# Kernel optimization log

Measured on AMD Instinct MI355X. Metric: run time of the kernel, lower is better.

Reference implementation:

```python
import jax, jax.numpy as jnp
import numpy as np

LATENT = 64
COND = 768
HEADS = 8
R = 8           # LoRA rank
SCALING = 1.0   # lora_alpha / r
SCALE = (LATENT / HEADS) ** -0.5


def _lora_linear(x, W, b, A, B):
    # loralib-style: y = x W^T + b + scaling * (x A^T) B^T
    return x @ W.T + b + SCALING * ((x @ A.T) @ B.T)


def setup_inputs() -> dict:
    key = jax.random.key(0)
    ks = jax.random.split(key, 20)
    B, C, H, W_ = 16, LATENT, 64, 64
    L = 77
    z = jax.random.normal(ks[0], (B, C, H, W_), dtype=jnp.float32)
    cond = jax.random.normal(ks[1], (B, L, COND), dtype=jnp.float32)

    def lin(k, out_d, in_d):
        k1, k2, k3 = jax.random.split(k, 3)
        W = jax.random.normal(k1, (out_d, in_d), dtype=jnp.float32) * 0.02
        b = jnp.zeros((out_d,), dtype=jnp.float32)
        A = jax.random.normal(k2, (R, in_d), dtype=jnp.float32) * 0.02
        Bm = jax.random.normal(k3, (out_d, R), dtype=jnp.float32) * 0.02
        return W, b, A, Bm

    Wq, bq, Aq, Bq = lin(ks[2], LATENT, LATENT)
    Wk, bk, Ak, Bk = lin(ks[3], LATENT, COND)
    Wv, bv, Av, Bv = lin(ks[4], LATENT, COND)
    Wo, bo, Ao, Bo = lin(ks[5], LATENT, LATENT)
    return dict(z=z, cond=cond,
                Wq=Wq, bq=bq, Aq=Aq, Bq=Bq,
                Wk=Wk, bk=bk, Ak=Ak, Bk=Bk,
                Wv=Wv, bv=bv, Av=Av, Bv=Bv,
                Wo=Wo, bo=bo, Ao=Ao, Bo=Bo)


def reference(z, cond, Wq, bq, Aq, Bq, Wk, bk, Ak, Bk, Wv, bv, Av, Bv, Wo, bo, Ao, Bo):
    B, C, H, W_ = z.shape
    hw = H * W_
    dh = C // HEADS
    z_flat = z.transpose(0, 2, 3, 1).reshape(B, hw, C)  # [B, hw, C]

    q = _lora_linear(z_flat, Wq, bq, Aq, Bq)   # [B, hw, C]
    k = _lora_linear(cond, Wk, bk, Ak, Bk)     # [B, L, C]
    v = _lora_linear(cond, Wv, bv, Av, Bv)     # [B, L, C]

    q = q.reshape(B, hw, HEADS, dh).transpose(0, 2, 1, 3)  # [B, h, hw, dh]
    k = k.reshape(B, -1, HEADS, dh).transpose(0, 2, 1, 3)  # [B, h, L, dh]
    v = v.reshape(B, -1, HEADS, dh).transpose(0, 2, 1, 3)

    dots = jnp.einsum('bhqd,bhkd->bhqk', q, k) * SCALE  # [B, h, hw, L]
    attn = jax.nn.softmax(dots, axis=-1)
    out = jnp.einsum('bhqk,bhkd->bhqd', attn, v)        # [B, h, hw, dh]
    out = out.transpose(0, 2, 1, 3).reshape(B, hw, C)
    out = _lora_linear(out, Wo, bo, Ao, Bo)
    return out.reshape(B, H, W_, C).transpose(0, 3, 1, 2)  # [B, C, H, W]
```

## Files before the change

### kernel.cpp

```cpp
#include <hip/hip_runtime.h>


#define HW   4096
#define CHN  64
#define LSEQ 77
#define CD   768
#define NB   16

#define OFF_WQ 0
#define OFF_WK 4096
#define OFF_WV 53248
#define OFF_WO 102400
#define OFF_K  106496
#define OFF_V  185344
#define OFF_PA 264192

#define QF 0.51011784563163f

__global__ __launch_bounds__(256) void prep_weights(
    const float* __restrict__ Wq, const float* __restrict__ Aq, const float* __restrict__ Bq,
    const float* __restrict__ Wk, const float* __restrict__ Ak, const float* __restrict__ Bk,
    const float* __restrict__ Wv, const float* __restrict__ Av, const float* __restrict__ Bv,
    const float* __restrict__ Wo, const float* __restrict__ Ao, const float* __restrict__ Bo,
    float* __restrict__ ws) {
  int idx = blockIdx.x * 256 + threadIdx.x;
  const float *W, *A, *Bm;
  float* out;
  int in_d, local;
  float scale = 1.0f;
  if (idx < 4096)        { W = Wq; A = Aq; Bm = Bq; out = ws + OFF_WQ; in_d = 64;  local = idx; scale = QF; }
  else if (idx < 53248)  { W = Wk; A = Ak; Bm = Bk; out = ws + OFF_WK; in_d = 768; local = idx - 4096; }
  else if (idx < 102400) { W = Wv; A = Av; Bm = Bv; out = ws + OFF_WV; in_d = 768; local = idx - 53248; }
  else                   { W = Wo; A = Ao; Bm = Bo; out = ws + OFF_WO; in_d = 64;  local = idx - 102400; }
  int co = local & 63;
  int c  = local >> 6;
  float val = W[co * in_d + c];
  #pragma unroll
  for (int r = 0; r < 8; r++) val += Bm[co * 8 + r] * A[r * in_d + c];
  out[local] = val * scale;
}

__global__ __launch_bounds__(128, 2) void kvproj(
    const float* __restrict__ cond,
    const float* __restrict__ wkT,
    const float* __restrict__ wvT,
    float* __restrict__ part) {
  int chunk = blockIdx.x;
  int kv    = blockIdx.y;
  int b     = blockIdx.z;
  int l     = threadIdx.x;
  if (l >= LSEQ) return;
  const float* wT = kv ? wvT : wkT;
  int c0 = chunk * 64;
  const float* xr = cond + (b * LSEQ + l) * CD + c0;
  float zr[64];
  #pragma unroll
  for (int i = 0; i < 16; i++) {
    float4 t4 = ((const float4*)xr)[i];
    zr[4*i] = t4.x; zr[4*i+1] = t4.y; zr[4*i+2] = t4.z; zr[4*i+3] = t4.w;
  }
  float acc[64];
  #pragma unroll
  for (int co = 0; co < 64; co++) acc[co] = 0.f;
  #pragma unroll 4
  for (int c = 0; c < 64; c++) {
    float zv = zr[c];
    #pragma unroll
    for (int co = 0; co < 64; co++) acc[co] = fmaf(zv, wT[(c0 + c) * 64 + co], acc[co]);
  }
  float* pout = part + (((kv * 12 + chunk) * NB + b) * LSEQ + l) * 64;
  #pragma unroll
  for (int i = 0; i < 16; i++) {
    ((float4*)pout)[i] = make_float4(acc[4*i], acc[4*i+1], acc[4*i+2], acc[4*i+3]);
  }
}

__global__ __launch_bounds__(256) void kvreduce(
    const float* __restrict__ part,
    const float* __restrict__ bk, const float* __restrict__ bv,
    float* __restrict__ kbuf, float* __restrict__ vbuf) {
  int idx = blockIdx.x * 256 + threadIdx.x;
  int kv = idx / (NB * LSEQ * 64);
  int r  = idx - kv * (NB * LSEQ * 64);
  int co = idx & 63;
  float val = kv ? bv[co] : bk[co];
  #pragma unroll
  for (int ch = 0; ch < 12; ch++)
    val += part[(kv * 12 + ch) * (NB * LSEQ * 64) + r];
  (kv ? vbuf : kbuf)[r] = val;
}

__global__ __launch_bounds__(256, 2) void megattn(
    const float* __restrict__ z,
    const float* __restrict__ wqT,
    const float* __restrict__ bq,
    const float* __restrict__ kbuf,
    const float* __restrict__ vbuf,
    const float* __restrict__ woT,
    const float* __restrict__ bo,
    float* __restrict__ out) {
  __shared__ float smem[LSEQ * 64 * 2];
  int b  = blockIdx.y;
  int p0 = blockIdx.x * 128;
  int t  = threadIdx.x;
  int h  = t >> 5;
  int pl = t & 31;

  float* ks = smem;
  float* vs = smem + LSEQ * 64;
  {
    const float4* ksrc = (const float4*)(kbuf + b * LSEQ * 64);
    const float4* vsrc = (const float4*)(vbuf + b * LSEQ * 64);
    float4* kd = (float4*)ks;
    float4* vd = (float4*)vs;
    for (int i = t; i < LSEQ * 16; i += 256) { kd[i] = ksrc[i]; vd[i] = vsrc[i]; }
  }

  float qr[4][8];
  {
    const float4 b0 = *(const float4*)(bq + 8 * h);
    const float4 b1 = *(const float4*)(bq + 8 * h + 4);
    #pragma unroll
    for (int i = 0; i < 4; i++) {
      qr[i][0] = b0.x * QF; qr[i][1] = b0.y * QF; qr[i][2] = b0.z * QF; qr[i][3] = b0.w * QF;
      qr[i][4] = b1.x * QF; qr[i][5] = b1.y * QF; qr[i][6] = b1.z * QF; qr[i][7] = b1.w * QF;
    }
  }
  const float* zb = z + b * (CHN * HW) + p0 + pl;
  #pragma unroll 4
  for (int c = 0; c < 64; c++) {
    float4 w0 = *(const float4*)(wqT + c * 64 + 8 * h);
    float4 w1 = *(const float4*)(wqT + c * 64 + 8 * h + 4);
    float zv[4];
    #pragma unroll
    for (int i = 0; i < 4; i++) zv[i] = zb[c * HW + 32 * i];
    #pragma unroll
    for (int i = 0; i < 4; i++) {
      qr[i][0] = fmaf(zv[i], w0.x, qr[i][0]);
      qr[i][1] = fmaf(zv[i], w0.y, qr[i][1]);
      qr[i][2] = fmaf(zv[i], w0.z, qr[i][2]);
      qr[i][3] = fmaf(zv[i], w0.w, qr[i][3]);
      qr[i][4] = fmaf(zv[i], w1.x, qr[i][4]);
      qr[i][5] = fmaf(zv[i], w1.y, qr[i][5]);
      qr[i][6] = fmaf(zv[i], w1.z, qr[i][6]);
      qr[i][7] = fmaf(zv[i], w1.w, qr[i][7]);
    }
  }
  __syncthreads();

  float acc[4][8];
  float li[4];
  #pragma unroll
  for (int i = 0; i < 4; i++) {
    li[i] = 0.f;
    #pragma unroll
    for (int d = 0; d < 8; d++) acc[i][d] = 0.f;
  }
  #pragma unroll 2
  for (int j = 0; j < LSEQ; j++) {
    float4 k0 = *(const float4*)(ks + j * 64 + 8 * h);
    float4 k1 = *(const float4*)(ks + j * 64 + 8 * h + 4);
    float4 v0 = *(const float4*)(vs + j * 64 + 8 * h);
    float4 v1 = *(const float4*)(vs + j * 64 + 8 * h + 4);
    #pragma unroll
    for (int i = 0; i < 4; i++) {
      float s = qr[i][0] * k0.x;
      s = fmaf(qr[i][1], k0.y, s);
      s = fmaf(qr[i][2], k0.z, s);
      s = fmaf(qr[i][3], k0.w, s);
      s = fmaf(qr[i][4], k1.x, s);
      s = fmaf(qr[i][5], k1.y, s);
      s = fmaf(qr[i][6], k1.z, s);
      s = fmaf(qr[i][7], k1.w, s);
      float e = __builtin_amdgcn_exp2f(s);
      li[i] += e;
      acc[i][0] = fmaf(e, v0.x, acc[i][0]);
      acc[i][1] = fmaf(e, v0.y, acc[i][1]);
      acc[i][2] = fmaf(e, v0.z, acc[i][2]);
      acc[i][3] = fmaf(e, v0.w, acc[i][3]);
      acc[i][4] = fmaf(e, v1.x, acc[i][4]);
      acc[i][5] = fmaf(e, v1.y, acc[i][5]);
      acc[i][6] = fmaf(e, v1.z, acc[i][6]);
      acc[i][7] = fmaf(e, v1.w, acc[i][7]);
    }
  }
  __syncthreads();

  float* ao = smem;
  #pragma unroll
  for (int i = 0; i < 4; i++) {
    float inv = 1.0f / li[i];
    int p = pl + 32 * i;
    #pragma unroll
    for (int d = 0; d < 8; d++) ao[p * 65 + 8 * h + d] = acc[i][d] * inv;
  }
  __syncthreads();

  int q2 = t & 127;
  int chalf = __builtin_amdgcn_readfirstlane((t >> 7) & 1);
  float acc2[32];
  #pragma unroll
  for (int j2 = 0; j2 < 32; j2++) acc2[j2] = bo[chalf * 32 + j2];
  const float* aor = ao + q2 * 65;
  #pragma unroll 4
  for (int c = 0; c < 64; c++) {
    float xv = aor[c];
    const float* wr = woT + c * 64 + chalf * 32;
    #pragma unroll
    for (int j2 = 0; j2 < 32; j2++) acc2[j2] = fmaf(xv, wr[j2], acc2[j2]);
  }
  float* ob = out + b * (CHN * HW) + p0 + q2;
  #pragma unroll
  for (int j2 = 0; j2 < 32; j2++) ob[(chalf * 32 + j2) * HW] = acc2[j2];
}

extern "C" void kernel_launch(void* const* d_in, const int* in_sizes, int n_in,
                              void* d_out, int out_size, void* d_ws, size_t ws_size,
                              hipStream_t stream) {
  const float* z    = (const float*)d_in[0];
  const float* cond = (const float*)d_in[1];
  const float* Wq = (const float*)d_in[2];  const float* bq = (const float*)d_in[3];
  const float* Aq = (const float*)d_in[4];  const float* Bq = (const float*)d_in[5];
  const float* Wk = (const float*)d_in[6];  const float* bk = (const float*)d_in[7];
  const float* Ak = (const float*)d_in[8];  const float* Bk = (const float*)d_in[9];
  const float* Wv = (const float*)d_in[10]; const float* bv = (const float*)d_in[11];
  const float* Av = (const float*)d_in[12]; const float* Bv = (const float*)d_in[13];
  const float* Wo = (const float*)d_in[14]; const float* bo = (const float*)d_in[15];
  const float* Ao = (const float*)d_in[16]; const float* Bo = (const float*)d_in[17];
  float* ws  = (float*)d_ws;
  float* out = (float*)d_out;

  prep_weights<<<416, 256, 0, stream>>>(Wq, Aq, Bq, Wk, Ak, Bk, Wv, Av, Bv, Wo, Ao, Bo, ws);
  kvproj<<<dim3(12, 2, 16), 128, 0, stream>>>(cond, ws + OFF_WK, ws + OFF_WV, ws + OFF_PA);
  kvreduce<<<616, 256, 0, stream>>>(ws + OFF_PA, bk, bv, ws + OFF_K, ws + OFF_V);
  megattn<<<dim3(32, 16), 256, 0, stream>>>(z, ws + OFF_WQ, bq, ws + OFF_K, ws + OFF_V,
                                            ws + OFF_WO, bo, out);
}
```

Before: 178.4 us.

## Double pixels per block in attention kernel and retile output projection per head

The fused attention kernel now handles 256 pixels per block instead of 128, so each thread keeps 8 query rows. This spreads the K/V shared-memory reads over twice as many rows. The output projection is reorganised so each thread computes 8 output channels for its 8 pixels, reading attention outputs from padded shared memory as float2. The grid halves to 256 blocks and the occupancy hint is dropped, so register pressure rises and there are fewer blocks to fill the GPU.

```diff
diff --git a/kernel.cpp b/kernel.cpp
--- a/kernel.cpp
+++ b/kernel.cpp
@@ -6,6 +6,7 @@
 #define LSEQ 77
 #define CD   768
 #define NB   16
+#define PAD  66
 
 #define OFF_WQ 0
 #define OFF_WK 4096
@@ -90,7 +91,7 @@
   (kv ? vbuf : kbuf)[r] = val;
 }
 
-__global__ __launch_bounds__(256, 2) void megattn(
+__global__ __launch_bounds__(256) void megattn(
     const float* __restrict__ z,
     const float* __restrict__ wqT,
     const float* __restrict__ bq,
@@ -99,12 +100,12 @@
     const float* __restrict__ woT,
     const float* __restrict__ bo,
     float* __restrict__ out) {
-  __shared__ float smem[LSEQ * 64 * 2];
+  __shared__ float smem[256 * PAD];
   int b  = blockIdx.y;
-  int p0 = blockIdx.x * 128;
+  int p0 = blockIdx.x * 256;
   int t  = threadIdx.x;
   int h  = t >> 5;
-  int pl = t & 31;
+  int l  = t & 31;
 
   float* ks = smem;
   float* vs = smem + LSEQ * 64;
@@ -116,42 +117,40 @@
     for (int i = t; i < LSEQ * 16; i += 256) { kd[i] = ksrc[i]; vd[i] = vsrc[i]; }
   }
 
-  float qr[4][8];
+  float q[8][8];
+  #pragma unroll
+  for (int i = 0; i < 8; i++)
+    #pragma unroll
+    for (int d = 0; d < 8; d++) q[i][d] = bq[8 * h + d] * QF;
   {
-    const float4 b0 = *(const float4*)(bq + 8 * h);
-    const float4 b1 = *(const float4*)(bq + 8 * h + 4);
-    #pragma unroll
-    for (int i = 0; i < 4; i++) {
-      qr[i][0] = b0.x * QF; qr[i][1] = b0.y * QF; qr[i][2] = b0.z * QF; qr[i][3] = b0.w * QF;
-      qr[i][4] = b1.x * QF; qr[i][5] = b1.y * QF; qr[i][6] = b1.z * QF; qr[i][7] = b1.w * QF;
+    const float* zb = z + b * (CHN * HW) + p0 + l;
+    const float* wq = wqT + 8 * h;
+    #pragma unroll 2
+    for (int c = 0; c < 64; c++) {
+      float zv[8];
+      #pragma unroll
+      for (int i = 0; i < 8; i++) zv[i] = zb[c * HW + 32 * i];
+      float4 w0 = *(const float4*)(wq + c * 64);
+      float4 w1 = *(const float4*)(wq + c * 64 + 4);
+      #pragma unroll
+      for (int i = 0; i < 8; i++) {
+        q[i][0] = fmaf(zv[i], w0.x, q[i][0]);
+        q[i][1] = fmaf(zv[i], w0.y, q[i][1]);
+        q[i][2] = fmaf(zv[i], w0.z, q[i][2]);
+        q[i][3] = fmaf(zv[i], w0.w, q[i][3]);
+        q[i][4] = fmaf(zv[i], w1.x, q[i][4]);
+        q[i][5] = fmaf(zv[i], w1.y, q[i][5]);
+        q[i][6] = fmaf(zv[i], w1.z, q[i][6]);
+        q[i][7] = fmaf(zv[i], w1.w, q[i][7]);
+      }
     }
   }
-  const float* zb = z + b * (CHN * HW) + p0 + pl;
-  #pragma unroll 4
-  for (int c = 0; c < 64; c++) {
-    float4 w0 = *(const float4*)(wqT + c * 64 + 8 * h);
-    float4 w1 = *(const float4*)(wqT + c * 64 + 8 * h + 4);
-    float zv[4];
-    #pragma unroll
-    for (int i = 0; i < 4; i++) zv[i] = zb[c * HW + 32 * i];
-    #pragma unroll
-    for (int i = 0; i < 4; i++) {
-      qr[i][0] = fmaf(zv[i], w0.x, qr[i][0]);
-      qr[i][1] = fmaf(zv[i], w0.y, qr[i][1]);
-      qr[i][2] = fmaf(zv[i], w0.z, qr[i][2]);
-      qr[i][3] = fmaf(zv[i], w0.w, qr[i][3]);
-      qr[i][4] = fmaf(zv[i], w1.x, qr[i][4]);
-      qr[i][5] = fmaf(zv[i], w1.y, qr[i][5]);
-      qr[i][6] = fmaf(zv[i], w1.z, qr[i][6]);
-      qr[i][7] = fmaf(zv[i], w1.w, qr[i][7]);
-    }
-  }
   __syncthreads();
 
-  float acc[4][8];
-  float li[4];
-  #pragma unroll
-  for (int i = 0; i < 4; i++) {
+  float acc[8][8];
+  float li[8];
+  #pragma unroll
+  for (int i = 0; i < 8; i++) {
     li[i] = 0.f;
     #pragma unroll
     for (int d = 0; d < 8; d++) acc[i][d] = 0.f;
@@ -163,16 +162,10 @@
     float4 v0 = *(const float4*)(vs + j * 64 + 8 * h);
     float4 v1 = *(const float4*)(vs + j * 64 + 8 * h + 4);
     #pragma unroll
-    for (int i = 0; i < 4; i++) {
-      float s = qr[i][0] * k0.x;
-      s = fmaf(qr[i][1], k0.y, s);
-      s = fmaf(qr[i][2], k0.z, s);
-      s = fmaf(qr[i][3], k0.w, s);
-      s = fmaf(qr[i][4], k1.x, s);
-      s = fmaf(qr[i][5], k1.y, s);
-      s = fmaf(qr[i][6], k1.z, s);
-      s = fmaf(qr[i][7], k1.w, s);
-      float e = __builtin_amdgcn_exp2f(s);
+    for (int i = 0; i < 8; i++) {
+      float sa = fmaf(q[i][3], k0.w, fmaf(q[i][2], k0.z, fmaf(q[i][1], k0.y, q[i][0] * k0.x)));
+      float sb = fmaf(q[i][7], k1.w, fmaf(q[i][6], k1.z, fmaf(q[i][5], k1.y, q[i][4] * k1.x)));
+      float e = __builtin_amdgcn_exp2f(sa + sb);
       li[i] += e;
       acc[i][0] = fmaf(e, v0.x, acc[i][0]);
       acc[i][1] = fmaf(e, v0.y, acc[i][1]);
@@ -188,30 +181,55 @@
 
   float* ao = smem;
   #pragma unroll
-  for (int i = 0; i < 4; i++) {
+  for (int i = 0; i < 8; i++) {
     float inv = 1.0f / li[i];
-    int p = pl + 32 * i;
-    #pragma unroll
-    for (int d = 0; d < 8; d++) ao[p * 65 + 8 * h + d] = acc[i][d] * inv;
+    float* aor = ao + (l + 32 * i) * PAD + 8 * h;
+    #pragma unroll
+    for (int d = 0; d < 8; d += 2)
+      *(float2*)(aor + d) = make_float2(acc[i][d] * inv, acc[i][d + 1] * inv);
   }
   __syncthreads();
 
-  int q2 = t & 127;
-  int chalf = __builtin_amdgcn_readfirstlane((t >> 7) & 1);
-  float acc2[32];
-  #pragma unroll
-  for (int j2 = 0; j2 < 32; j2++) acc2[j2] = bo[chalf * 32 + j2];
-  const float* aor = ao + q2 * 65;
-  #pragma unroll 4
-  for (int c = 0; c < 64; c++) {
-    float xv = aor[c];
-    const float* wr = woT + c * 64 + chalf * 32;
-    #pragma unroll
-    for (int j2 = 0; j2 < 32; j2++) acc2[j2] = fmaf(xv, wr[j2], acc2[j2]);
-  }
-  float* ob = out + b * (CHN * HW) + p0 + q2;
-  #pragma unroll
-  for (int j2 = 0; j2 < 32; j2++) ob[(chalf * 32 + j2) * HW] = acc2[j2];
+  {
+    float o[8][8];
+    #pragma unroll
+    for (int i = 0; i < 8; i++)
+      #pragma unroll
+      for (int d = 0; d < 8; d++) o[i][d] = bo[8 * h + d];
+    const float* wo = woT + 8 * h;
+    #pragma unroll 2
+    for (int c = 0; c < 64; c += 2) {
+      float4 w0 = *(const float4*)(wo + c * 64);
+      float4 w1 = *(const float4*)(wo + c * 64 + 4);
+      float4 w2 = *(const float4*)(wo + (c + 1) * 64);
+      float4 w3 = *(const float4*)(wo + (c + 1) * 64 + 4);
+      #pragma unroll
+      for (int i = 0; i < 8; i++) {
+        float2 a2 = *(const float2*)(ao + (l + 32 * i) * PAD + c);
+        o[i][0] = fmaf(a2.x, w0.x, o[i][0]);
+        o[i][1] = fmaf(a2.x, w0.y, o[i][1]);
+        o[i][2] = fmaf(a2.x, w0.z, o[i][2]);
+        o[i][3] = fmaf(a2.x, w0.w, o[i][3]);
+        o[i][4] = fmaf(a2.x, w1.x, o[i][4]);
+        o[i][5] = fmaf(a2.x, w1.y, o[i][5]);
+        o[i][6] = fmaf(a2.x, w1.z, o[i][6]);
+        o[i][7] = fmaf(a2.x, w1.w, o[i][7]);
+        o[i][0] = fmaf(a2.y, w2.x, o[i][0]);
+        o[i][1] = fmaf(a2.y, w2.y, o[i][1]);
+        o[i][2] = fmaf(a2.y, w2.z, o[i][2]);
+        o[i][3] = fmaf(a2.y, w2.w, o[i][3]);
+        o[i][4] = fmaf(a2.y, w3.x, o[i][4]);
+        o[i][5] = fmaf(a2.y, w3.y, o[i][5]);
+        o[i][6] = fmaf(a2.y, w3.z, o[i][6]);
+        o[i][7] = fmaf(a2.y, w3.w, o[i][7]);
+      }
+    }
+    float* ob = out + b * (CHN * HW) + p0 + l;
+    #pragma unroll
+    for (int i = 0; i < 8; i++)
+      #pragma unroll
+      for (int d = 0; d < 8; d++) ob[(8 * h + d) * HW + 32 * i] = o[i][d];
+  }
 }
 
 extern "C" void kernel_launch(void* const* d_in, const int* in_sizes, int n_in,
@@ -233,6 +251,6 @@
   prep_weights<<<416, 256, 0, stream>>>(Wq, Aq, Bq, Wk, Ak, Bk, Wv, Av, Bv, Wo, Ao, Bo, ws);
   kvproj<<<dim3(12, 2, 16), 128, 0, stream>>>(cond, ws + OFF_WK, ws + OFF_WV, ws + OFF_PA);
   kvreduce<<<616, 256, 0, stream>>>(ws + OFF_PA, bk, bv, ws + OFF_K, ws + OFF_V);
-  megattn<<<dim3(32, 16), 256, 0, stream>>>(z, ws + OFF_WQ, bq, ws + OFF_K, ws + OFF_V,
+  megattn<<<dim3(16, 16), 256, 0, stream>>>(z, ws + OFF_WQ, bq, ws + OFF_K, ws + OFF_V,
                                             ws + OFF_WO, bo, out);
 }
```

After: 183.7 us. 3.0% more time.
